# Optimization experiments

Hardware: AMD Instinct MI355X
Metric: run time of the kernel (lower is better)

## Reference

```python
import jax, jax.numpy as jnp
import numpy as np


def setup_inputs() -> dict:
    key = jax.random.key(0)
    k1, k2, k3 = jax.random.split(key, 3)
    B, S, H, E = 4, 4096, 7168, 256
    return {
        "hidden_states": jax.random.normal(k1, (B, S, H), dtype=jnp.float32),
        "gate_weight": jax.random.normal(k2, (E, H), dtype=jnp.float32) * (H ** -0.5),
        "bias": jax.random.normal(k3, (E,), dtype=jnp.float32) * 0.01,
        "n_group": 8,
        "topk_group": 4,
        "top_k": 8,
    }


def reference(hidden_states, gate_weight, bias, n_group, topk_group, top_k):
    B, S, H = hidden_states.shape
    E = gate_weight.shape[0]
    group_size = E // n_group
    x = hidden_states.reshape(-1, H)  # [T, H]
    logits = jnp.einsum("th,eh->te", x, gate_weight)  # [T, E]
    scores = jax.nn.sigmoid(logits) + bias  # [T, E]
    scores_g = scores.reshape(-1, n_group, group_size)  # [T, G, E/G]
    group_scores = scores_g.max(axis=-1)  # [T, G]
    _, sel_groups = jax.lax.top_k(group_scores, topk_group)  # [T, topk_group]
    # group mask: 1.0 for selected groups (indices are distinct, so sum of one-hots is 0/1)
    group_mask = jax.nn.one_hot(sel_groups, n_group, dtype=scores.dtype).sum(axis=1)  # [T, G]
    masked = (scores_g * group_mask[:, :, None]).reshape(-1, E)  # [T, E]
    weights, indices = jax.lax.top_k(masked, top_k)  # [T, top_k]
    weights = weights / (weights.sum(axis=-1, keepdims=True) + 1e-6)
    return weights.reshape(B, S, -1), indices.reshape(B, S, -1)
```

## Files before the change

kernel.cpp:

```cpp
#include <hip/hip_runtime.h>


#define TTOK 16384
#define EEXP 256
#define HDIM 7168
#define BM 64
#define BK 64
#define NSTEP (HDIM / BK)
#define NTHR 512
#define LDS_BYTES 163840
#define ABASE 131072

typedef __attribute__((ext_vector_type(4))) float f32x4;
typedef __attribute__((ext_vector_type(8))) _Float16 h8;

__device__ __forceinline__ void gload_lds16(const void* g, void* l) {
  typedef const __attribute__((address_space(1))) unsigned int gu32;
  typedef __attribute__((address_space(3))) unsigned int lu32;
  __builtin_amdgcn_global_load_lds((gu32*)g, (lu32*)l, 16, 0, 0);
}

__global__ __launch_bounds__(64) void pack_w_kernel(const float* __restrict__ W,
                                                    _Float16* __restrict__ blob) {
  const int kcg = blockIdx.x;
  const int eb = blockIdx.y;
  const int lane = threadIdx.x;
  const int e = eb * 16 + (lane & 15);
  const int k0 = kcg * 32 + (lane >> 4) * 8;
  const float* src = W + (size_t)e * HDIM + k0;
  h8 hi, lo;
#pragma unroll
  for (int j = 0; j < 8; ++j) {
    float x = src[j];
    _Float16 h = (_Float16)x;
    hi[j] = h;
    lo[j] = (_Float16)((x - (float)h) * 2048.0f);
  }
  char* dst = (char*)blob + ((size_t)kcg * 32 + eb * 2) * 1024 + lane * 16;
  *(h8*)dst = hi;
  *(h8*)(dst + 1024) = lo;
}

__global__ __launch_bounds__(NTHR, 1) void gate_kernel(
    const float* __restrict__ X, const _Float16* __restrict__ Wblob,
    const float* __restrict__ bias, float* __restrict__ outw,
    float* __restrict__ outi) {
  extern __shared__ char smem[];
  float (*scores)[EEXP + 1] = (float (*)[EEXP + 1])smem;

  const int tid = threadIdx.x;
  const int lane = tid & 63;
  const int wid = tid >> 6;
  const int wr = wid >> 2;
  const int wc = wid & 3;
  const int tok0 = blockIdx.x * BM;

  const int arow = tid >> 3, ac8 = tid & 7;
  const float* asrc = X + (size_t)(tok0 + arow) * HDIM + ac8 * 8;
  const int awoff = arow * 128 + ((ac8 ^ (arow & 7)) << 4);

  f32x4 ra0, ra1;

  f32x4 acc1[2][4], acc2[2][4];
#pragma unroll
  for (int m = 0; m < 2; ++m)
#pragma unroll
    for (int n = 0; n < 4; ++n) {
      acc1[m][n] = (f32x4){0.f, 0.f, 0.f, 0.f};
      acc2[m][n] = (f32x4){0.f, 0.f, 0.f, 0.f};
    }

  auto LOADA = [&](int step) {
    ra0 = *(const f32x4*)(asrc + (size_t)step * BK);
    ra1 = *(const f32x4*)(asrc + (size_t)step * BK + 4);
  };

  auto STAGEB = [&](int step, int buf) {
    const char* gs = (const char*)Wblob + (size_t)step * 65536 + lane * 16;
    char* lb = smem + buf * 65536;
#pragma unroll
    for (int i = 0; i < 8; ++i) {
      const int gb = i * 8 + wid;
      gload_lds16(gs + gb * 1024, lb + gb * 1024);
    }
  };

  auto ACONV = [&](int buf) {
    h8 hi, lo;
#pragma unroll
    for (int j = 0; j < 4; ++j) {
      float x = ra0[j];
      _Float16 h = (_Float16)x;
      hi[j] = h;
      lo[j] = (_Float16)((x - (float)h) * 2048.0f);
      float y = ra1[j];
      _Float16 g = (_Float16)y;
      hi[4 + j] = g;
      lo[4 + j] = (_Float16)((y - (float)g) * 2048.0f);
    }
    char* ab = smem + ABASE + buf * 16384;
    *(h8*)(ab + awoff) = hi;
    *(h8*)(ab + 8192 + awoff) = lo;
  };

#define PHASE(S, BUF)                                                           \
  {                                                                             \
    const char* ab = smem + ABASE + (BUF) * 16384;                              \
    const char* bb = smem + (BUF) * 65536;                                      \
    h8 ah[2], al[2];                                                            \
    _Pragma("unroll") for (int m = 0; m < 2; ++m) {                             \
      const int r_ = wr * 32 + m * 16 + (lane & 15);                            \
      const int ao_ = r_ * 128 + ((((S) * 4 + (lane >> 4)) ^ (lane & 7)) << 4); \
      ah[m] = *(const h8*)(ab + ao_);                                           \
      al[m] = *(const h8*)(ab + 8192 + ao_);                                    \
    }                                                                           \
    h8 bh[4], bl[4];                                                            \
    _Pragma("unroll") for (int n = 0; n < 4; ++n) {                             \
      const int bo_ = (((S) * 16 + (wc * 4 + n)) * 2) * 1024 + lane * 16;       \
      bh[n] = *(const h8*)(bb + bo_);                                           \
      bl[n] = *(const h8*)(bb + bo_ + 1024);                                    \
    }                                                                           \
    _Pragma("unroll") for (int n = 0; n < 4; ++n)                               \
        _Pragma("unroll") for (int m = 0; m < 2; ++m) {                         \
      acc1[m][n] = __builtin_amdgcn_mfma_f32_16x16x32_f16(ah[m], bh[n], acc1[m][n], 0, 0, 0); \
      acc2[m][n] = __builtin_amdgcn_mfma_f32_16x16x32_f16(ah[m], bl[n], acc2[m][n], 0, 0, 0); \
      acc2[m][n] = __builtin_amdgcn_mfma_f32_16x16x32_f16(al[m], bh[n], acc2[m][n], 0, 0, 0); \
    }                                                                           \
  }

  LOADA(0);
  STAGEB(0, 0);
  ACONV(0);
  asm volatile("s_waitcnt vmcnt(0) lgkmcnt(0)" ::: "memory");
  __builtin_amdgcn_s_barrier();

  int buf = 0;
#pragma unroll 1
  for (int kk = 0; kk < NSTEP; ++kk) {
    const bool pf = (kk + 1 < NSTEP);
    if (pf) {
      LOADA(kk + 1);
      STAGEB(kk + 1, buf ^ 1);
    }
    PHASE(0, buf);
    PHASE(1, buf);
    if (pf) ACONV(buf ^ 1);
    asm volatile("s_waitcnt vmcnt(0) lgkmcnt(0)" ::: "memory");
    __builtin_amdgcn_s_barrier();
    buf ^= 1;
  }

#pragma unroll
  for (int m = 0; m < 2; ++m)
#pragma unroll
    for (int n = 0; n < 4; ++n) {
      const int e = (wc * 4 + n) * 16 + (lane & 15);
      const float b = bias[e];
      const int t0 = wr * 32 + m * 16 + (lane >> 4) * 4;
#pragma unroll
      for (int r = 0; r < 4; ++r) {
        const float logit = acc1[m][n][r] + acc2[m][n][r] * (1.0f / 2048.0f);
        scores[t0 + r][e] = 1.0f / (1.0f + expf(-logit)) + b;
      }
    }
  __syncthreads();

  if ((lane & 7) == 0) {
    const int t = wid * 8 + (lane >> 3);
    const float* sc = scores[t];

    float gmax[8];
#pragma unroll
    for (int g = 0; g < 8; ++g) {
      float mx = -1e30f;
      for (int j = 0; j < 32; ++j) mx = fmaxf(mx, sc[g * 32 + j]);
      gmax[g] = mx;
    }
    unsigned selmask = 0;
    for (int it = 0; it < 4; ++it) {
      float best = -1e30f;
      int bi = 0;
      for (int g = 0; g < 8; ++g)
        if (!((selmask >> g) & 1) && gmax[g] > best) {
          best = gmax[g];
          bi = g;
        }
      selmask |= 1u << bi;
    }
    float vals[8];
    int idx[8];
#pragma unroll
    for (int j = 0; j < 8; ++j) {
      vals[j] = -1e30f;
      idx[j] = 0;
    }
    for (int e = 0; e < 256; ++e) {
      const float v = ((selmask >> (e >> 5)) & 1) ? sc[e] : 0.0f;
      if (v > vals[7]) {
        int p = 7;
        while (p > 0 && v > vals[p - 1]) {
          vals[p] = vals[p - 1];
          idx[p] = idx[p - 1];
          --p;
        }
        vals[p] = v;
        idx[p] = e;
      }
    }
    float ssum = 0.0f;
#pragma unroll
    for (int j = 0; j < 8; ++j) ssum += vals[j];
    const float den = ssum + 1e-6f;
    const long tg = (long)tok0 + t;
#pragma unroll
    for (int j = 0; j < 8; ++j) {
      outw[tg * 8 + j] = vals[j] / den;
      outi[tg * 8 + j] = (float)idx[j];
    }
  }
}

extern "C" void kernel_launch(void* const* d_in, const int* in_sizes, int n_in,
                              void* d_out, int out_size, void* d_ws, size_t ws_size,
                              hipStream_t stream) {
  const float* X = (const float*)d_in[0];
  const float* W = (const float*)d_in[1];
  const float* bias = (const float*)d_in[2];

  _Float16* wblob = (_Float16*)d_ws;

  float* outw = (float*)d_out;
  float* outi = outw + (size_t)TTOK * 8;

  hipFuncSetAttribute((const void*)gate_kernel,
                      hipFuncAttributeMaxDynamicSharedMemorySize, LDS_BYTES);

  pack_w_kernel<<<dim3(HDIM / 32, EEXP / 16), 64, 0, stream>>>(W, wblob);
  gate_kernel<<<TTOK / BM, NTHR, LDS_BYTES, stream>>>(X, wblob, bias, outw, outi);
}
```

Measured before the change: 285.7 us.

## Split-K GEMM with larger token tiles, XCD-aware slicing and separate epilogue

The token tile doubles to 128 rows per block and the hidden dimension is split into two K-slices. Block IDs are mapped so that each XCD group works on one slice, which is meant to keep each slice's weight blob in its own L2. Partial logits go to a global workspace, and a new epilogue kernel sums them and applies sigmoid, bias and the grouped top-k. The A tile is now single-buffered with an extra barrier, the waitcnt is partial, and MFMA priority is raised. In exchange it adds a round trip of partial logits through global memory, a third kernel launch and more registers for the larger accumulator set.

```diff
diff --git a/kernel.cpp b/kernel.cpp
--- a/kernel.cpp
+++ b/kernel.cpp
@@ -4,12 +4,15 @@
 #define TTOK 16384
 #define EEXP 256
 #define HDIM 7168
-#define BM 64
+#define BM 128
 #define BK 64
-#define NSTEP (HDIM / BK)
+#define SPLITK 2
+#define KSLICE (HDIM / SPLITK)
+#define NSTEP (KSLICE / BK)
 #define NTHR 512
 #define LDS_BYTES 163840
 #define ABASE 131072
+#define EPI_LDS (64 * 257 * 4)
 
 typedef __attribute__((ext_vector_type(4))) float f32x4;
 typedef __attribute__((ext_vector_type(8))) _Float16 h8;
@@ -41,42 +44,45 @@
   *(h8*)(dst + 1024) = lo;
 }
 
-__global__ __launch_bounds__(NTHR, 1) void gate_kernel(
+__global__ __launch_bounds__(NTHR, 2) void gate_kernel(
     const float* __restrict__ X, const _Float16* __restrict__ Wblob,
-    const float* __restrict__ bias, float* __restrict__ outw,
-    float* __restrict__ outi) {
+    float* __restrict__ part) {
   extern __shared__ char smem[];
-  float (*scores)[EEXP + 1] = (float (*)[EEXP + 1])smem;
+
+  const int bid = blockIdx.x;
+  const int xcd = bid & 7;
+  const int slice = xcd >> 2;
+  const int tb = ((bid >> 3) << 2) | (bid & 3);
+  const int tok0 = tb * BM;
+  const int kbase = slice * KSLICE;
+  const char* blobs = (const char*)Wblob + (size_t)slice * (KSLICE / 32) * 32768;
 
   const int tid = threadIdx.x;
   const int lane = tid & 63;
   const int wid = tid >> 6;
   const int wr = wid >> 2;
   const int wc = wid & 3;
-  const int tok0 = blockIdx.x * BM;
-
-  const int arow = tid >> 3, ac8 = tid & 7;
-  const float* asrc = X + (size_t)(tok0 + arow) * HDIM + ac8 * 8;
-  const int awoff = arow * 128 + ((ac8 ^ (arow & 7)) << 4);
-
-  f32x4 ra0, ra1;
-
-  f32x4 acc1[2][4], acc2[2][4];
-#pragma unroll
-  for (int m = 0; m < 2; ++m)
+
+  f32x4 ra[4];
+
+  f32x4 acc1[4][4], acc2[4][4];
+#pragma unroll
+  for (int m = 0; m < 4; ++m)
 #pragma unroll
     for (int n = 0; n < 4; ++n) {
       acc1[m][n] = (f32x4){0.f, 0.f, 0.f, 0.f};
       acc2[m][n] = (f32x4){0.f, 0.f, 0.f, 0.f};
     }
 
-  auto LOADA = [&](int step) {
-    ra0 = *(const f32x4*)(asrc + (size_t)step * BK);
-    ra1 = *(const f32x4*)(asrc + (size_t)step * BK + 4);
+  auto LOADA = [&](int T) {
+    const float* p = X + (size_t)(tok0 + (tid >> 2)) * HDIM + kbase + T * BK +
+                     (tid & 3) * 16;
+#pragma unroll
+    for (int i = 0; i < 4; ++i) ra[i] = *(const f32x4*)(p + i * 4);
   };
 
-  auto STAGEB = [&](int step, int buf) {
-    const char* gs = (const char*)Wblob + (size_t)step * 65536 + lane * 16;
+  auto STAGEB = [&](int T, int buf) {
+    const char* gs = blobs + (size_t)T * 65536 + lane * 16;
     char* lb = smem + buf * 65536;
 #pragma unroll
     for (int i = 0; i < 8; ++i) {
@@ -85,34 +91,43 @@
     }
   };
 
-  auto ACONV = [&](int buf) {
-    h8 hi, lo;
-#pragma unroll
-    for (int j = 0; j < 4; ++j) {
-      float x = ra0[j];
-      _Float16 h = (_Float16)x;
-      hi[j] = h;
-      lo[j] = (_Float16)((x - (float)h) * 2048.0f);
-      float y = ra1[j];
-      _Float16 g = (_Float16)y;
-      hi[4 + j] = g;
-      lo[4 + j] = (_Float16)((y - (float)g) * 2048.0f);
-    }
-    char* ab = smem + ABASE + buf * 16384;
-    *(h8*)(ab + awoff) = hi;
-    *(h8*)(ab + 8192 + awoff) = lo;
+  auto STOREA = [&]() {
+    const int row = tid >> 2, q = tid & 3;
+    char* abh = smem + ABASE;
+    char* abl = smem + ABASE + 16384;
+#pragma unroll
+    for (int c = 0; c < 2; ++c) {
+      h8 hi, lo;
+#pragma unroll
+      for (int half = 0; half < 2; ++half) {
+        const f32x4 v = (half == 0) ? ra[2 * c] : ra[2 * c + 1];
+#pragma unroll
+        for (int j = 0; j < 4; ++j) {
+          const float x = v[j];
+          const _Float16 h = (_Float16)x;
+          hi[half * 4 + j] = h;
+          lo[half * 4 + j] = (_Float16)((x - (float)h) * 2048.0f);
+        }
+      }
+      const int cc = q * 2 + c;
+      const int ix = row * 128 + ((cc ^ (row & 7)) << 4);
+      *(h8*)(abh + ix) = hi;
+      *(h8*)(abl + ix) = lo;
+    }
   };
 
 #define PHASE(S, BUF)                                                           \
   {                                                                             \
-    const char* ab = smem + ABASE + (BUF) * 16384;                              \
+    const char* abh = smem + ABASE;                                             \
+    const char* abl = smem + ABASE + 16384;                                     \
     const char* bb = smem + (BUF) * 65536;                                      \
-    h8 ah[2], al[2];                                                            \
-    _Pragma("unroll") for (int m = 0; m < 2; ++m) {                             \
-      const int r_ = wr * 32 + m * 16 + (lane & 15);                            \
-      const int ao_ = r_ * 128 + ((((S) * 4 + (lane >> 4)) ^ (lane & 7)) << 4); \
-      ah[m] = *(const h8*)(ab + ao_);                                           \
-      al[m] = *(const h8*)(ab + 8192 + ao_);                                    \
+    h8 ah[4], al[4];                                                            \
+    _Pragma("unroll") for (int m = 0; m < 4; ++m) {                             \
+      const int r_ = wr * 64 + m * 16 + (lane & 15);                            \
+      const int c_ = ((S) * 4 + (lane >> 4)) ^ (r_ & 7);                        \
+      const int ao_ = r_ * 128 + (c_ << 4);                                     \
+      ah[m] = *(const h8*)(abh + ao_);                                          \
+      al[m] = *(const h8*)(abl + ao_);                                          \
     }                                                                           \
     h8 bh[4], bl[4];                                                            \
     _Pragma("unroll") for (int n = 0; n < 4; ++n) {                             \
@@ -120,60 +135,88 @@
       bh[n] = *(const h8*)(bb + bo_);                                           \
       bl[n] = *(const h8*)(bb + bo_ + 1024);                                    \
     }                                                                           \
+    __builtin_amdgcn_s_setprio(1);                                              \
     _Pragma("unroll") for (int n = 0; n < 4; ++n)                               \
-        _Pragma("unroll") for (int m = 0; m < 2; ++m) {                         \
+        _Pragma("unroll") for (int m = 0; m < 4; ++m) {                         \
       acc1[m][n] = __builtin_amdgcn_mfma_f32_16x16x32_f16(ah[m], bh[n], acc1[m][n], 0, 0, 0); \
       acc2[m][n] = __builtin_amdgcn_mfma_f32_16x16x32_f16(ah[m], bl[n], acc2[m][n], 0, 0, 0); \
       acc2[m][n] = __builtin_amdgcn_mfma_f32_16x16x32_f16(al[m], bh[n], acc2[m][n], 0, 0, 0); \
     }                                                                           \
+    __builtin_amdgcn_s_setprio(0);                                              \
   }
 
   LOADA(0);
+  asm volatile("" ::: "memory");
   STAGEB(0, 0);
-  ACONV(0);
+  STOREA();
   asm volatile("s_waitcnt vmcnt(0) lgkmcnt(0)" ::: "memory");
   __builtin_amdgcn_s_barrier();
 
   int buf = 0;
 #pragma unroll 1
-  for (int kk = 0; kk < NSTEP; ++kk) {
-    const bool pf = (kk + 1 < NSTEP);
+  for (int T = 0; T < NSTEP; ++T) {
+    const bool pf = (T + 1 < NSTEP);
     if (pf) {
-      LOADA(kk + 1);
-      STAGEB(kk + 1, buf ^ 1);
+      STAGEB(T + 1, buf ^ 1);
+      asm volatile("" ::: "memory");
+      LOADA(T + 1);
     }
     PHASE(0, buf);
     PHASE(1, buf);
-    if (pf) ACONV(buf ^ 1);
-    asm volatile("s_waitcnt vmcnt(0) lgkmcnt(0)" ::: "memory");
+    if (pf) asm volatile("s_waitcnt vmcnt(4)" ::: "memory");
     __builtin_amdgcn_s_barrier();
+    if (pf) {
+      STOREA();
+      asm volatile("s_waitcnt lgkmcnt(0)" ::: "memory");
+      __builtin_amdgcn_s_barrier();
+    }
     buf ^= 1;
   }
 
-#pragma unroll
-  for (int m = 0; m < 2; ++m)
+  float* pbase = part + ((size_t)slice * TTOK + tok0) * EEXP;
+#pragma unroll
+  for (int m = 0; m < 4; ++m)
 #pragma unroll
     for (int n = 0; n < 4; ++n) {
-      const int e = (wc * 4 + n) * 16 + (lane & 15);
-      const float b = bias[e];
-      const int t0 = wr * 32 + m * 16 + (lane >> 4) * 4;
-#pragma unroll
-      for (int r = 0; r < 4; ++r) {
-        const float logit = acc1[m][n][r] + acc2[m][n][r] * (1.0f / 2048.0f);
-        scores[t0 + r][e] = 1.0f / (1.0f + expf(-logit)) + b;
-      }
-    }
+      const int e = wc * 64 + n * 16 + (lane & 15);
+      const int t0 = wr * 64 + m * 16 + (lane >> 4) * 4;
+#pragma unroll
+      for (int r = 0; r < 4; ++r)
+        pbase[(size_t)(t0 + r) * EEXP + e] =
+            acc1[m][n][r] + acc2[m][n][r] * (1.0f / 2048.0f);
+    }
+}
+
+__global__ __launch_bounds__(256) void epilogue_kernel(
+    const float* __restrict__ part, const float* __restrict__ bias,
+    float* __restrict__ outw, float* __restrict__ outi) {
+  extern __shared__ float sc[];
+  const int tid = threadIdx.x;
+  const long t0 = (long)blockIdx.x * 64;
+
+  const int e4 = (tid & 63) * 4;
+  const int rsub = tid >> 6;
+  const f32x4 bv = *(const f32x4*)(bias + e4);
+#pragma unroll
+  for (int rr = 0; rr < 16; ++rr) {
+    const int row = rr * 4 + rsub;
+    const f32x4 a = *(const f32x4*)(part + (t0 + row) * EEXP + e4);
+    const f32x4 c = *(const f32x4*)(part + ((long)TTOK + t0 + row) * EEXP + e4);
+#pragma unroll
+    for (int j = 0; j < 4; ++j) {
+      const float v = a[j] + c[j];
+      sc[row * 257 + e4 + j] = 1.0f / (1.0f + expf(-v)) + bv[j];
+    }
+  }
   __syncthreads();
 
-  if ((lane & 7) == 0) {
-    const int t = wid * 8 + (lane >> 3);
-    const float* sc = scores[t];
-
+  if (tid < 64) {
+    const float* s = sc + tid * 257;
     float gmax[8];
 #pragma unroll
     for (int g = 0; g < 8; ++g) {
       float mx = -1e30f;
-      for (int j = 0; j < 32; ++j) mx = fmaxf(mx, sc[g * 32 + j]);
+      for (int j = 0; j < 32; ++j) mx = fmaxf(mx, s[g * 32 + j]);
       gmax[g] = mx;
     }
     unsigned selmask = 0;
@@ -195,7 +238,7 @@
       idx[j] = 0;
     }
     for (int e = 0; e < 256; ++e) {
-      const float v = ((selmask >> (e >> 5)) & 1) ? sc[e] : 0.0f;
+      const float v = ((selmask >> (e >> 5)) & 1) ? s[e] : 0.0f;
       if (v > vals[7]) {
         int p = 7;
         while (p > 0 && v > vals[p - 1]) {
@@ -211,7 +254,7 @@
 #pragma unroll
     for (int j = 0; j < 8; ++j) ssum += vals[j];
     const float den = ssum + 1e-6f;
-    const long tg = (long)tok0 + t;
+    const long tg = t0 + tid;
 #pragma unroll
     for (int j = 0; j < 8; ++j) {
       outw[tg * 8 + j] = vals[j] / den;
@@ -228,13 +271,17 @@
   const float* bias = (const float*)d_in[2];
 
   _Float16* wblob = (_Float16*)d_ws;
+  float* part = (float*)((char*)d_ws + (size_t)EEXP * HDIM * 4);
 
   float* outw = (float*)d_out;
   float* outi = outw + (size_t)TTOK * 8;
 
   hipFuncSetAttribute((const void*)gate_kernel,
                       hipFuncAttributeMaxDynamicSharedMemorySize, LDS_BYTES);
+  hipFuncSetAttribute((const void*)epilogue_kernel,
+                      hipFuncAttributeMaxDynamicSharedMemorySize, EPI_LDS);
 
   pack_w_kernel<<<dim3(HDIM / 32, EEXP / 16), 64, 0, stream>>>(W, wblob);
-  gate_kernel<<<TTOK / BM, NTHR, LDS_BYTES, stream>>>(X, wblob, bias, outw, outi);
-}
+  gate_kernel<<<SPLITK * (TTOK / BM), NTHR, LDS_BYTES, stream>>>(X, wblob, part);
+  epilogue_kernel<<<TTOK / 64, 256, EPI_LDS, stream>>>(part, bias, outw, outi);
+}
```

Result: no change. 290.0 us (+1.5%).

## Triple-buffer W tiles with BK=32 and split-phase MFMA pipeline with priority hints

Applied to the files above, without the earlier changes.

Halves the K step to 32 and triple-buffers the W tile in LDS, staging two steps ahead in two halves interleaved with the MFMA clusters. The A tile uses a padded plane layout in place of the XOR swizzle, and vmcnt waits are made partial so global loads stay in flight across steps. s_setprio is raised around MFMA clusters. The aim is to hide load latency behind compute, at the cost of more barriers per step and tighter waitcnt bookkeeping.

```diff
diff --git a/kernel.cpp b/kernel.cpp
--- a/kernel.cpp
+++ b/kernel.cpp
@@ -5,13 +5,16 @@
 #define EEXP 256
 #define HDIM 7168
 #define BM 64
-#define BK 64
-#define NSTEP (HDIM / BK)
+#define BK 32
+#define NKC (HDIM / BK)
 #define NTHR 512
-#define LDS_BYTES 163840
-#define ABASE 131072
+#define BBASE(i) ((i) * 32768)
+#define ABASE 98304
+#define APLANE 4160
+#define LDS_BYTES 114944
 
 typedef __attribute__((ext_vector_type(4))) float f32x4;
+typedef __attribute__((ext_vector_type(4))) _Float16 h4;
 typedef __attribute__((ext_vector_type(8))) _Float16 h8;
 
 __device__ __forceinline__ void gload_lds16(const void* g, void* l) {
@@ -55,11 +58,11 @@
   const int wc = wid & 3;
   const int tok0 = blockIdx.x * BM;
 
-  const int arow = tid >> 3, ac8 = tid & 7;
-  const float* asrc = X + (size_t)(tok0 + arow) * HDIM + ac8 * 8;
-  const int awoff = arow * 128 + ((ac8 ^ (arow & 7)) << 4);
-
-  f32x4 ra0, ra1;
+  const int arow = tid >> 3, aq = tid & 7;
+  const float* asrc = X + (size_t)(tok0 + arow) * HDIM + aq * 4;
+  const int awoff = (aq >> 1) * 1040 + arow * 16 + (aq & 1) * 8;
+
+  f32x4 ra;
 
   f32x4 acc1[2][4], acc2[2][4];
 #pragma unroll
@@ -70,91 +73,100 @@
       acc2[m][n] = (f32x4){0.f, 0.f, 0.f, 0.f};
     }
 
-  auto LOADA = [&](int step) {
-    ra0 = *(const f32x4*)(asrc + (size_t)step * BK);
-    ra1 = *(const f32x4*)(asrc + (size_t)step * BK + 4);
+  auto LOADA = [&](int T) { ra = *(const f32x4*)(asrc + (size_t)T * BK); };
+
+  auto STAGEB2 = [&](int T, int buf, int half) {
+    const char* gs = (const char*)Wblob + (size_t)T * 32768 + lane * 16;
+    char* lb = smem + BBASE(buf) + lane * 16;
+    const int g0 = wid * 4 + half * 2;
+    gload_lds16(gs + g0 * 1024, lb + g0 * 1024);
+    gload_lds16(gs + (g0 + 1) * 1024, lb + (g0 + 1) * 1024);
   };
 
-  auto STAGEB = [&](int step, int buf) {
-    const char* gs = (const char*)Wblob + (size_t)step * 65536 + lane * 16;
-    char* lb = smem + buf * 65536;
-#pragma unroll
-    for (int i = 0; i < 8; ++i) {
-      const int gb = i * 8 + wid;
-      gload_lds16(gs + gb * 1024, lb + gb * 1024);
-    }
-  };
-
-  auto ACONV = [&](int buf) {
-    h8 hi, lo;
+  auto ACONV = [&](int abuf) {
+    h4 hi, lo;
 #pragma unroll
     for (int j = 0; j < 4; ++j) {
-      float x = ra0[j];
-      _Float16 h = (_Float16)x;
+      const float x = ra[j];
+      const _Float16 h = (_Float16)x;
       hi[j] = h;
       lo[j] = (_Float16)((x - (float)h) * 2048.0f);
-      float y = ra1[j];
-      _Float16 g = (_Float16)y;
-      hi[4 + j] = g;
-      lo[4 + j] = (_Float16)((y - (float)g) * 2048.0f);
-    }
-    char* ab = smem + ABASE + buf * 16384;
-    *(h8*)(ab + awoff) = hi;
-    *(h8*)(ab + 8192 + awoff) = lo;
+    }
+    char* ap = smem + ABASE + abuf * (2 * APLANE);
+    *(h4*)(ap + awoff) = hi;
+    *(h4*)(ap + APLANE + awoff) = lo;
   };
 
-#define PHASE(S, BUF)                                                           \
+#define MFMA_CLUSTER(NH, BB_, AHH, ALL)                                         \
   {                                                                             \
-    const char* ab = smem + ABASE + (BUF) * 16384;                              \
-    const char* bb = smem + (BUF) * 65536;                                      \
-    h8 ah[2], al[2];                                                            \
-    _Pragma("unroll") for (int m = 0; m < 2; ++m) {                             \
-      const int r_ = wr * 32 + m * 16 + (lane & 15);                            \
-      const int ao_ = r_ * 128 + ((((S) * 4 + (lane >> 4)) ^ (lane & 7)) << 4); \
-      ah[m] = *(const h8*)(ab + ao_);                                           \
-      al[m] = *(const h8*)(ab + 8192 + ao_);                                    \
+    __builtin_amdgcn_s_setprio(1);                                              \
+    _Pragma("unroll") for (int n2 = 0; n2 < 2; ++n2) {                          \
+      const int n_ = (NH) * 2 + n2;                                             \
+      const int bo_ = ((wc * 4 + n_) * 2) * 1024 + lane * 16;                   \
+      const h8 bh = *(const h8*)((BB_) + bo_);                                  \
+      const h8 bl = *(const h8*)((BB_) + bo_ + 1024);                           \
+      _Pragma("unroll") for (int m = 0; m < 2; ++m) {                           \
+        acc1[m][n_] = __builtin_amdgcn_mfma_f32_16x16x32_f16(AHH[m], bh, acc1[m][n_], 0, 0, 0); \
+        acc2[m][n_] = __builtin_amdgcn_mfma_f32_16x16x32_f16(AHH[m], bl, acc2[m][n_], 0, 0, 0); \
+        acc2[m][n_] = __builtin_amdgcn_mfma_f32_16x16x32_f16(ALL[m], bh, acc2[m][n_], 0, 0, 0); \
+      }                                                                         \
     }                                                                           \
-    h8 bh[4], bl[4];                                                            \
-    _Pragma("unroll") for (int n = 0; n < 4; ++n) {                             \
-      const int bo_ = (((S) * 16 + (wc * 4 + n)) * 2) * 1024 + lane * 16;       \
-      bh[n] = *(const h8*)(bb + bo_);                                           \
-      bl[n] = *(const h8*)(bb + bo_ + 1024);                                    \
-    }                                                                           \
-    _Pragma("unroll") for (int n = 0; n < 4; ++n)                               \
-        _Pragma("unroll") for (int m = 0; m < 2; ++m) {                         \
-      acc1[m][n] = __builtin_amdgcn_mfma_f32_16x16x32_f16(ah[m], bh[n], acc1[m][n], 0, 0, 0); \
-      acc2[m][n] = __builtin_amdgcn_mfma_f32_16x16x32_f16(ah[m], bl[n], acc2[m][n], 0, 0, 0); \
-      acc2[m][n] = __builtin_amdgcn_mfma_f32_16x16x32_f16(al[m], bh[n], acc2[m][n], 0, 0, 0); \
-    }                                                                           \
-  }
-
+    __builtin_amdgcn_s_setprio(0);                                              \
+  }
+
+  STAGEB2(0, 0, 0);
+  STAGEB2(0, 0, 1);
+  STAGEB2(1, 1, 0);
+  STAGEB2(1, 1, 1);
   LOADA(0);
-  STAGEB(0, 0);
   ACONV(0);
-  asm volatile("s_waitcnt vmcnt(0) lgkmcnt(0)" ::: "memory");
+  LOADA(1);
+  asm volatile("s_waitcnt vmcnt(5) lgkmcnt(0)" ::: "memory");
   __builtin_amdgcn_s_barrier();
 
-  int buf = 0;
+  int pb = 0;
 #pragma unroll 1
-  for (int kk = 0; kk < NSTEP; ++kk) {
-    const bool pf = (kk + 1 < NSTEP);
-    if (pf) {
-      LOADA(kk + 1);
-      STAGEB(kk + 1, buf ^ 1);
-    }
-    PHASE(0, buf);
-    PHASE(1, buf);
-    if (pf) ACONV(buf ^ 1);
-    asm volatile("s_waitcnt vmcnt(0) lgkmcnt(0)" ::: "memory");
-    __builtin_amdgcn_s_barrier();
-    buf ^= 1;
-  }
+  for (int T = 0; T < NKC; ++T) {
+    const int pa = T & 1;
+    const bool p2 = (T + 2 < NKC);
+    const char* ap = smem + ABASE + pa * (2 * APLANE);
+    const char* bb = smem + BBASE(pb);
+
+    h8 ahf[2], alf[2];
+#pragma unroll
+    for (int m = 0; m < 2; ++m) {
+      const int r_ = wr * 32 + m * 16 + (lane & 15);
+      const int ao_ = (lane >> 4) * 1040 + r_ * 16;
+      ahf[m] = *(const h8*)(ap + ao_);
+      alf[m] = *(const h8*)(ap + APLANE + ao_);
+    }
+    if (p2) STAGEB2(T + 2, (T + 2) % 3, 0);
+    __builtin_amdgcn_s_barrier();
+    MFMA_CLUSTER(0, bb, ahf, alf);
+    __builtin_amdgcn_s_barrier();
+
+    if (p2) STAGEB2(T + 2, (T + 2) % 3, 1);
+    if (T + 1 < NKC) ACONV(pa ^ 1);
+    if (p2) LOADA(T + 2);
+    asm volatile("s_waitcnt lgkmcnt(0)" ::: "memory");
+    if (p2)
+      asm volatile("s_waitcnt vmcnt(5)" ::: "memory");
+    else
+      asm volatile("s_waitcnt vmcnt(0)" ::: "memory");
+    __builtin_amdgcn_s_barrier();
+    MFMA_CLUSTER(1, bb, ahf, alf);
+    __builtin_amdgcn_s_barrier();
+
+    pb = (pb == 2) ? 0 : pb + 1;
+  }
+
+  __syncthreads();
 
 #pragma unroll
   for (int m = 0; m < 2; ++m)
 #pragma unroll
     for (int n = 0; n < 4; ++n) {
-      const int e = (wc * 4 + n) * 16 + (lane & 15);
+      const int e = wc * 64 + n * 16 + (lane & 15);
       const float b = bias[e];
       const int t0 = wr * 32 + m * 16 + (lane >> 4) * 4;
 #pragma unroll
@@ -235,6 +247,6 @@
   hipFuncSetAttribute((const void*)gate_kernel,
                       hipFuncAttributeMaxDynamicSharedMemorySize, LDS_BYTES);
 
-  pack_w_kernel<<<dim3(HDIM / 32, EEXP / 16), 64, 0, stream>>>(W, wblob);
+  pack_w_kernel<<<dim3(NKC, EEXP / 16), 64, 0, stream>>>(W, wblob);
   gate_kernel<<<TTOK / BM, NTHR, LDS_BYTES, stream>>>(X, wblob, bias, outw, outi);
 }
```

Result: slower. 390.6 us (+36.7%).
